# Performance work log

Hardware: AMD Instinct MI355X
Metric: run time of the kernel (lower is better)

Reference implementation:

```python
import jax, jax.numpy as jnp
import numpy as np

N, E = 100000, 1600000
IN, ED, H, HL, OUT = 32, 8, 16, 64, 4
BN_EPS = 1e-5


def setup_inputs() -> dict:
    key = jax.random.key(0)
    keys = iter(jax.random.split(key, 64))

    def rn(*s):
        return jax.random.normal(next(keys), s, jnp.float32) * 0.1

    inp = {}
    inp["x"] = jax.random.normal(next(keys), (N, IN), jnp.float32)
    inp["edge_index"] = jax.random.randint(next(keys), (2, E), 0, N)
    inp["edge_attr"] = jax.random.normal(next(keys), (E, ED), jnp.float32)
    for c, din in ((1, IN), (2, H), (3, H)):
        inp[f"ew{c}"] = rn(ED, din)   # GINEConv edge lin: edge_dim -> in_channels
        inp[f"eb{c}"] = rn(din)
        inp[f"wa{c}"] = rn(din, H)    # nn Linear 1
        inp[f"ba{c}"] = rn(H)
        inp[f"g{c}"] = jnp.ones((H,), jnp.float32)    # BN gamma
        inp[f"be{c}"] = jnp.zeros((H,), jnp.float32)  # BN beta
        inp[f"m{c}"] = rn(H)                           # BN running mean
        inp[f"v{c}"] = jax.random.uniform(next(keys), (H,), jnp.float32, 0.5, 1.5)  # BN running var
        inp[f"wb{c}"] = rn(H, H)      # nn Linear 2
        inp[f"bb{c}"] = rn(H)
    inp["lw1"] = rn(3 * H, HL)
    inp["lb1"] = rn(HL)
    inp["lw2"] = rn(HL, OUT)
    inp["lb2"] = rn(OUT)
    return inp


def gine_conv(x, edge_attr, src, dst, ew, eb, wa, ba, g, be, m, v, wb, bb):
    # message: relu(x_j + lin_edge(edge_attr)); aggregate: sum at dst; eps = 0
    e = edge_attr @ ew + eb                      # [E, din]
    msg = jax.nn.relu(x[src] + e)                # [E, din]
    agg = jax.ops.segment_sum(msg, dst, num_segments=x.shape[0])  # [N, din]
    h = (x + agg) @ wa + ba                      # Linear 1
    h = (h - m) * jax.lax.rsqrt(v + BN_EPS) * g + be  # BatchNorm1d (eval)
    h = jax.nn.relu(h)
    h = jax.nn.relu(h @ wb + bb)                 # Linear 2 + ReLU
    return h


def reference(x, edge_index, edge_attr,
              ew1, eb1, wa1, ba1, g1, be1, m1, v1, wb1, bb1,
              ew2, eb2, wa2, ba2, g2, be2, m2, v2, wb2, bb2,
              ew3, eb3, wa3, ba3, g3, be3, m3, v3, wb3, bb3,
              lw1, lb1, lw2, lb2):
    src, dst = edge_index[0], edge_index[1]
    h1 = gine_conv(x, edge_attr, src, dst, ew1, eb1, wa1, ba1, g1, be1, m1, v1, wb1, bb1)
    h2 = gine_conv(h1, edge_attr, src, dst, ew2, eb2, wa2, ba2, g2, be2, m2, v2, wb2, bb2)
    h3 = gine_conv(h2, edge_attr, src, dst, ew3, eb3, wa3, ba3, g3, be3, m3, v3, wb3, bb3)
    h = jnp.concatenate((h1, h2, h3), axis=1)    # [N, 3H]
    h = jax.nn.relu(h @ lw1 + lb1)               # dropout p=0.5 is identity in eval
    return h @ lw2 + lb2                         # [N, OUT]
```

## Files before the change

kernel.cpp:

```cpp
#include <hip/hip_runtime.h>
#include <hip/hip_bf16.h>

#define BN_EPS 1e-5f
#define BINSHIFT 6
#define BINW 64
#define NBLK 1024

__device__ __forceinline__ unsigned pk_bf16(float x, float y) {
    unsigned ux = __float_as_uint(x);
    ux += 0x7FFFu + ((ux >> 16) & 1u);
    unsigned uy = __float_as_uint(y);
    uy += 0x7FFFu + ((uy >> 16) & 1u);
    return (ux >> 16) | (uy & 0xFFFF0000u);
}
__device__ __forceinline__ float bf_lo(unsigned u) { return __uint_as_float(u << 16); }
__device__ __forceinline__ float bf_hi(unsigned u) { return __uint_as_float(u & 0xFFFF0000u); }

__device__ __forceinline__ int chunk_of(int bid) {
    return ((bid & 7) << 7) | (bid >> 3);
}


__global__ __launch_bounds__(256)
void hist2d_kernel(const int* __restrict__ dst, int* __restrict__ histmat,
                   int E, int nbins, int chunk) {
    __shared__ int h[2048];
    for (int i = threadIdx.x; i < nbins; i += 256) h[i] = 0;
    __syncthreads();
    int c = chunk_of(blockIdx.x);
    int e0 = c * chunk;
    int e1 = min(E, e0 + chunk);
    for (int e = e0 + threadIdx.x; e < e1; e += 256)
        atomicAdd(&h[dst[e] >> BINSHIFT], 1);
    __syncthreads();
    int* row = histmat + (size_t)c * nbins;
    for (int i = threadIdx.x; i < nbins; i += 256) row[i] = h[i];
}

__global__ __launch_bounds__(256)
void colsum_kernel(const int* __restrict__ histmat, int* __restrict__ bincnt,
                   int nbins) {
    int bin = blockIdx.x * 256 + threadIdx.x;
    if (bin >= nbins) return;
    int s = 0;
#pragma unroll 8
    for (int r = 0; r < NBLK; ++r) s += histmat[(size_t)r * nbins + bin];
    bincnt[bin] = s;
}

__global__ __launch_bounds__(1024)
void bin_scan_kernel(const int* __restrict__ bincnt, int* __restrict__ binstart,
                     int nbins, int E) {
    __shared__ int a[2048];
    __shared__ int b[1024];
    int t = threadIdx.x;
    a[t]        = (t < nbins) ? bincnt[t] : 0;
    a[t + 1024] = (t + 1024 < nbins) ? bincnt[t + 1024] : 0;
    __syncthreads();
    b[t] = a[2 * t] + a[2 * t + 1];
    __syncthreads();
    for (int off = 1; off < 1024; off <<= 1) {
        int v = (t >= off) ? b[t - off] : 0;
        __syncthreads();
        b[t] += v;
        __syncthreads();
    }
    int base = (t == 0) ? 0 : b[t - 1];
    if (2 * t < nbins)     binstart[2 * t]     = base;
    if (2 * t + 1 < nbins) binstart[2 * t + 1] = base + a[2 * t];
    if (t == 0) binstart[nbins] = E;
}

__global__ __launch_bounds__(1024)
void rowscan_kernel(int* __restrict__ histmat, const int* __restrict__ binstart,
                    int nbins) {
    __shared__ int a[NBLK];
    int b = blockIdx.x;
    int t = threadIdx.x;
    int v = histmat[(size_t)t * nbins + b];
    a[t] = v;
    __syncthreads();
    for (int off = 1; off < NBLK; off <<= 1) {
        int add = (t >= off) ? a[t - off] : 0;
        __syncthreads();
        a[t] += add;
        __syncthreads();
    }
    histmat[(size_t)t * nbins + b] = binstart[b] + a[t] - v;
}

__global__ __launch_bounds__(256)
void place_kernel(const int* __restrict__ src, const int* __restrict__ dst,
                  const float* __restrict__ edge_attr,
                  const int* __restrict__ histmat,
                  int* __restrict__ tmp_meta, uint4* __restrict__ tmp_ea,
                  int E, int nbins, int chunk) {
    __shared__ int cur[2048];
    int c = chunk_of(blockIdx.x);
    const int* row = histmat + (size_t)c * nbins;
    for (int i = threadIdx.x; i < nbins; i += 256) cur[i] = row[i];
    __syncthreads();
    int e0 = c * chunk;
    int e1 = min(E, e0 + chunk);
    for (int e = e0 + threadIdx.x; e < e1; e += 256) {
        int d = dst[e];
        int bin = d >> BINSHIFT;
        int pos = atomicAdd(&cur[bin], 1);
        tmp_meta[pos] = ((d & (BINW - 1)) << 20) | src[e];
        const float4* sp = (const float4*)(edge_attr + (size_t)e * 8);
        float4 a0 = sp[0], a1 = sp[1];
        uint4 pkd;
        pkd.x = pk_bf16(a0.x, a0.y);
        pkd.y = pk_bf16(a0.z, a0.w);
        pkd.z = pk_bf16(a1.x, a1.y);
        pkd.w = pk_bf16(a1.z, a1.w);
        tmp_ea[pos] = pkd;
    }
}

__global__ __launch_bounds__(256)
void pass2_kernel(const int* __restrict__ binstart, const int* __restrict__ tmp_meta,
                  const uint4* __restrict__ tmp_ea,
                  int* __restrict__ rowstart, int* __restrict__ src_sorted,
                  uint4* __restrict__ ea_sorted, int N, int E) {
    __shared__ int s_cur[BINW];
    int b = blockIdx.x;
    int node0 = b << BINSHIFT;
    int e0 = binstart[b], e1 = binstart[b + 1];
    int t = threadIdx.x;

    if (t < BINW) s_cur[t] = 0;
    __syncthreads();

    for (int e = e0 + t; e < e1; e += 256)
        atomicAdd(&s_cur[tmp_meta[e] >> 20], 1);
    __syncthreads();

    if (t < BINW) {
        int val = s_cur[t];
        int inc = val;
#pragma unroll
        for (int off = 1; off < 64; off <<= 1) {
            int n = __shfl_up(inc, off);
            if (t >= off) inc += n;
        }
        int excl = e0 + inc - val;
        s_cur[t] = excl;
        int node = node0 + t;
        if (node <= N) rowstart[node] = excl;
    }
    __syncthreads();

    for (int e = e0 + t; e < e1; e += 256) {
        int mx = tmp_meta[e];
        int dl   = mx >> 20;
        int srcv = mx & 0xFFFFF;
        int fpos = atomicAdd(&s_cur[dl], 1);
        src_sorted[fpos] = srcv;
        ea_sorted[fpos] = tmp_ea[e];
    }
}

template<int DIN, int C, int S>
__global__ __launch_bounds__(256)
void gine_layer_wave(const float* __restrict__ xin,
                     const int*   __restrict__ rowstart,
                     const int*   __restrict__ src_sorted,
                     const uint4* __restrict__ ea_sorted,
                     const float* __restrict__ ew, const float* __restrict__ eb,
                     const float* __restrict__ wa, const float* __restrict__ ba,
                     const float* __restrict__ g, const float* __restrict__ be,
                     const float* __restrict__ m, const float* __restrict__ v,
                     const float* __restrict__ wb, const float* __restrict__ bb,
                     float* __restrict__ hout,
                     int N) {
    static_assert(C * S == 64 && C * 4 == DIN, "lane layout");
    constexpr int PAD = DIN + 1;

    __shared__ float s_wa[DIN * 16];
    __shared__ float s_wb[256];
    __shared__ float s_ba[16], s_scale[16], s_shift[16], s_bb[16];
    __shared__ float s_s[16 * PAD];
    __shared__ float s_h[16 * 17];

    int t = threadIdx.x;
    for (int idx = t; idx < DIN * 16; idx += 256) s_wa[idx] = wa[idx];
    s_wb[t] = wb[t];
    if (t < 16) {
        s_ba[t] = ba[t];
        float sc = g[t] * rsqrtf(v[t] + BN_EPS);
        s_scale[t] = sc;
        s_shift[t] = be[t] - m[t] * sc;
        s_bb[t] = bb[t];
    }

    int w    = t >> 6;
    int lane = t & 63;
    int c    = lane / S;
    int s    = lane % S;
    int c0   = c * 4;

    float ew_r[8][4];
#pragma unroll
    for (int k = 0; k < 8; ++k) {
        float4 wv = *(const float4*)(ew + k * DIN + c0);
        ew_r[k][0] = wv.x; ew_r[k][1] = wv.y; ew_r[k][2] = wv.z; ew_r[k][3] = wv.w;
    }
    float4 ebv = *(const float4*)(eb + c0);
    float eb_r[4] = {ebv.x, ebv.y, ebv.z, ebv.w};

    int node0 = blockIdx.x * 16;

#pragma unroll
    for (int q = 0; q < 4; ++q) {
        int nl = w * 4 + q;
        int i  = node0 + nl;
        float acc[4] = {0.f, 0.f, 0.f, 0.f};
        if (i < N) {
            int e0 = rowstart[i];
            int e1 = rowstart[i + 1];
            int e  = e0 + s;
            int sv = (e < e1) ? src_sorted[e] : 0;
            for (; e < e1; e += S) {
                int en = e + S;
                int sv_next = (en < e1) ? src_sorted[en] : 0;
                uint4 ev = ea_sorted[e];
                float4 xv = *(const float4*)(xin + (size_t)sv * DIN + c0);
                float av[8] = {bf_lo(ev.x), bf_hi(ev.x), bf_lo(ev.y), bf_hi(ev.y),
                               bf_lo(ev.z), bf_hi(ev.z), bf_lo(ev.w), bf_hi(ev.w)};
                float xr[4] = {xv.x, xv.y, xv.z, xv.w};
#pragma unroll
                for (int j = 0; j < 4; ++j) {
                    float lin = eb_r[j];
#pragma unroll
                    for (int k = 0; k < 8; ++k) lin = fmaf(av[k], ew_r[k][j], lin);
                    lin += xr[j];
                    acc[j] += (lin > 0.f ? lin : 0.f);
                }
                sv = sv_next;
            }
        }
#pragma unroll
        for (int mask = S >> 1; mask >= 1; mask >>= 1) {
#pragma unroll
            for (int j = 0; j < 4; ++j) acc[j] += __shfl_xor(acc[j], mask);
        }
        if (s == 0 && i < N) {
            float4 xi = *(const float4*)(xin + (size_t)i * DIN + c0);
            s_s[nl * PAD + c0 + 0] = acc[0] + xi.x;
            s_s[nl * PAD + c0 + 1] = acc[1] + xi.y;
            s_s[nl * PAD + c0 + 2] = acc[2] + xi.z;
            s_s[nl * PAD + c0 + 3] = acc[3] + xi.w;
        }
    }
    __syncthreads();

    int nl2 = t >> 4;
    int j   = t & 15;
    float a = s_ba[j];
#pragma unroll
    for (int k = 0; k < DIN; ++k)
        a = fmaf(s_s[nl2 * PAD + k], s_wa[k * 16 + j], a);
    a = a * s_scale[j] + s_shift[j];
    s_h[nl2 * 17 + j] = a > 0.f ? a : 0.f;
    __syncthreads();

    float o = s_bb[j];
#pragma unroll
    for (int k = 0; k < 16; ++k)
        o = fmaf(s_h[nl2 * 17 + k], s_wb[k * 16 + j], o);
    o = o > 0.f ? o : 0.f;
    int i2 = node0 + nl2;
    if (i2 < N) hout[(size_t)i2 * 16 + j] = o;
}

__global__ __launch_bounds__(256)
void final_kernel(const float* __restrict__ h1, const float* __restrict__ h2,
                  const float* __restrict__ h3,
                  const float* __restrict__ lw1, const float* __restrict__ lb1,
                  const float* __restrict__ lw2, const float* __restrict__ lb2,
                  float* __restrict__ out, int N) {
    constexpr int NPB = 64;
    __shared__ float s_lw1[48 * 64];
    __shared__ float s_lw2[64 * 4];
    __shared__ float s_lb1[64];
    __shared__ float s_lb2[4];
    __shared__ float s_c[NPB][49];

    int t = threadIdx.x;
    for (int idx = t; idx < 48 * 64; idx += 256) s_lw1[idx] = lw1[idx];
    s_lw2[t] = lw2[t];
    if (t < 64) s_lb1[t] = lb1[t];
    if (t < 4) s_lb2[t] = lb2[t];

    int nl = t >> 2;
    int l  = t & 3;
    int i  = blockIdx.x * NPB + nl;

    if (i < N) {
        float4 c1 = ((const float4*)(h1 + (size_t)i * 16))[l];
        float4 c2 = ((const float4*)(h2 + (size_t)i * 16))[l];
        float4 c3 = ((const float4*)(h3 + (size_t)i * 16))[l];
        s_c[nl][l * 4 + 0] = c1.x; s_c[nl][l * 4 + 1] = c1.y;
        s_c[nl][l * 4 + 2] = c1.z; s_c[nl][l * 4 + 3] = c1.w;
        s_c[nl][16 + l * 4 + 0] = c2.x; s_c[nl][16 + l * 4 + 1] = c2.y;
        s_c[nl][16 + l * 4 + 2] = c2.z; s_c[nl][16 + l * 4 + 3] = c2.w;
        s_c[nl][32 + l * 4 + 0] = c3.x; s_c[nl][32 + l * 4 + 1] = c3.y;
        s_c[nl][32 + l * 4 + 2] = c3.z; s_c[nl][32 + l * 4 + 3] = c3.w;
    }
    __syncthreads();

    float o0 = 0.f, o1 = 0.f, o2 = 0.f, o3 = 0.f;
    if (i < N) {
#pragma unroll 4
        for (int jj = 0; jj < 16; ++jj) {
            int j = l * 16 + jj;
            float a = s_lb1[j];
#pragma unroll
            for (int k = 0; k < 48; ++k) a = fmaf(s_c[nl][k], s_lw1[k * 64 + j], a);
            a = a > 0.f ? a : 0.f;
            o0 = fmaf(a, s_lw2[j * 4 + 0], o0);
            o1 = fmaf(a, s_lw2[j * 4 + 1], o1);
            o2 = fmaf(a, s_lw2[j * 4 + 2], o2);
            o3 = fmaf(a, s_lw2[j * 4 + 3], o3);
        }
    }
    o0 += __shfl_xor(o0, 1); o0 += __shfl_xor(o0, 2);
    o1 += __shfl_xor(o1, 1); o1 += __shfl_xor(o1, 2);
    o2 += __shfl_xor(o2, 1); o2 += __shfl_xor(o2, 2);
    o3 += __shfl_xor(o3, 1); o3 += __shfl_xor(o3, 2);
    if (i < N && l == 0) {
        float4 o = {o0 + s_lb2[0], o1 + s_lb2[1], o2 + s_lb2[2], o3 + s_lb2[3]};
        *(float4*)(out + (size_t)i * 4) = o;
    }
}

extern "C" void kernel_launch(void* const* d_in, const int* in_sizes, int n_in,
                              void* d_out, int out_size, void* d_ws, size_t ws_size,
                              hipStream_t stream) {
    const float* x  = (const float*)d_in[0];
    const int*   ei = (const int*)d_in[1];
    const float* ea = (const float*)d_in[2];
    const int N = in_sizes[0] / 32;
    const int E = in_sizes[1] / 2;
    const int* srci = ei;
    const int* dsti = ei + E;

    const float* lw1 = (const float*)d_in[33];
    const float* lb1 = (const float*)d_in[34];
    const float* lw2 = (const float*)d_in[35];
    const float* lb2 = (const float*)d_in[36];

    const int nbins = (N + BINW - 1) >> BINSHIFT;
    const int chunk = (E + NBLK - 1) / NBLK;

    char* p = (char*)d_ws;
    int*   binstart   = (int*)p;   p += (size_t)(nbins + 1 + 3) / 4 * 16;
    int*   bincnt     = (int*)p;   p += (size_t)(nbins + 3) / 4 * 16;
    int*   rowstart   = (int*)p;   p += (size_t)(N + 1 + 3) / 4 * 16;
    int*   histmat    = (int*)p;   p += (size_t)NBLK * nbins * 4;
    int*   src_sorted = (int*)p;   p += (size_t)E * 4;
    uint4* ea_sorted  = (uint4*)p; p += (size_t)E * 16;
    char*  u          = p;
    int*   tmp_meta   = (int*)u;
    uint4* tmp_ea     = (uint4*)(u + (size_t)E * 4);
    float* h1         = (float*)u;
    float* h2         = h1 + (size_t)N * 16;
    float* h3         = h2 + (size_t)N * 16;

    hist2d_kernel<<<NBLK, 256, 0, stream>>>(dsti, histmat, E, nbins, chunk);
    colsum_kernel<<<(nbins + 255) / 256, 256, 0, stream>>>(histmat, bincnt, nbins);
    bin_scan_kernel<<<1, 1024, 0, stream>>>(bincnt, binstart, nbins, E);
    rowscan_kernel<<<nbins, NBLK, 0, stream>>>(histmat, binstart, nbins);
    place_kernel<<<NBLK, 256, 0, stream>>>(srci, dsti, ea, histmat,
                                           tmp_meta, tmp_ea, E, nbins, chunk);
    pass2_kernel<<<nbins, 256, 0, stream>>>(binstart, tmp_meta, tmp_ea,
                                            rowstart, src_sorted, ea_sorted,
                                            N, E);

    const int lblocks = (N + 15) / 16;
    gine_layer_wave<32, 8, 8><<<lblocks, 256, 0, stream>>>(
        x, rowstart, src_sorted, ea_sorted,
        (const float*)d_in[3], (const float*)d_in[4],
        (const float*)d_in[5], (const float*)d_in[6],
        (const float*)d_in[7], (const float*)d_in[8],
        (const float*)d_in[9], (const float*)d_in[10],
        (const float*)d_in[11], (const float*)d_in[12], h1, N);

    gine_layer_wave<16, 4, 16><<<lblocks, 256, 0, stream>>>(
        h1, rowstart, src_sorted, ea_sorted,
        (const float*)d_in[13], (const float*)d_in[14],
        (const float*)d_in[15], (const float*)d_in[16],
        (const float*)d_in[17], (const float*)d_in[18],
        (const float*)d_in[19], (const float*)d_in[20],
        (const float*)d_in[21], (const float*)d_in[22], h2, N);

    gine_layer_wave<16, 4, 16><<<lblocks, 256, 0, stream>>>(
        h2, rowstart, src_sorted, ea_sorted,
        (const float*)d_in[23], (const float*)d_in[24],
        (const float*)d_in[25], (const float*)d_in[26],
        (const float*)d_in[27], (const float*)d_in[28],
        (const float*)d_in[29], (const float*)d_in[30],
        (const float*)d_in[31], (const float*)d_in[32], h3, N);

    final_kernel<<<(N + 63) / 64, 256, 0, stream>>>(
        h1, h2, h3, lw1, lb1, lw2, lb2, (float*)d_out, N);
}
```

Measured before the change: 519.4 us.

## Transpose block histogram for segmented column scan; store layer outputs as bf16

```diff
diff --git a/kernel.cpp b/kernel.cpp
--- a/kernel.cpp
+++ b/kernel.cpp
@@ -5,6 +5,8 @@
 #define BINSHIFT 6
 #define BINW 64
 #define NBLK 1024
+#define NSEG 8
+#define SEGW (NBLK / NSEG)
 
 __device__ __forceinline__ unsigned pk_bf16(float x, float y) {
     unsigned ux = __float_as_uint(x);
@@ -13,6 +15,14 @@
     uy += 0x7FFFu + ((uy >> 16) & 1u);
     return (ux >> 16) | (uy & 0xFFFF0000u);
 }
+__device__ __forceinline__ unsigned short f2bf(float x) {
+    unsigned u = __float_as_uint(x);
+    u += 0x7FFFu + ((u >> 16) & 1u);
+    return (unsigned short)(u >> 16);
+}
+__device__ __forceinline__ float bfu(unsigned short u) {
+    return __uint_as_float((unsigned)u << 16);
+}
 __device__ __forceinline__ float bf_lo(unsigned u) { return __uint_as_float(u << 16); }
 __device__ __forceinline__ float bf_hi(unsigned u) { return __uint_as_float(u & 0xFFFF0000u); }
 
@@ -22,7 +32,7 @@
 
 
 __global__ __launch_bounds__(256)
-void hist2d_kernel(const int* __restrict__ dst, int* __restrict__ histmat,
+void hist2d_kernel(const int* __restrict__ dst, int* __restrict__ histmatT,
                    int E, int nbins, int chunk) {
     __shared__ int h[2048];
     for (int i = threadIdx.x; i < nbins; i += 256) h[i] = 0;
@@ -33,19 +43,26 @@
     for (int e = e0 + threadIdx.x; e < e1; e += 256)
         atomicAdd(&h[dst[e] >> BINSHIFT], 1);
     __syncthreads();
-    int* row = histmat + (size_t)c * nbins;
-    for (int i = threadIdx.x; i < nbins; i += 256) row[i] = h[i];
-}
-
-__global__ __launch_bounds__(256)
-void colsum_kernel(const int* __restrict__ histmat, int* __restrict__ bincnt,
-                   int nbins) {
+    for (int i = threadIdx.x; i < nbins; i += 256)
+        histmatT[(size_t)i * NBLK + c] = h[i];
+}
+
+__global__ __launch_bounds__(256)
+void colsum_kernel(const int* __restrict__ histmatT, int* __restrict__ bincnt,
+                   int* __restrict__ segsum, int nbins) {
     int bin = blockIdx.x * 256 + threadIdx.x;
     if (bin >= nbins) return;
-    int s = 0;
-#pragma unroll 8
-    for (int r = 0; r < NBLK; ++r) s += histmat[(size_t)r * nbins + bin];
-    bincnt[bin] = s;
+    const int* col = histmatT + (size_t)bin * NBLK;
+    int tot = 0;
+#pragma unroll
+    for (int s = 0; s < NSEG; ++s) {
+        int ps = 0;
+#pragma unroll 16
+        for (int r = 0; r < SEGW; ++r) ps += col[s * SEGW + r];
+        segsum[s * nbins + bin] = ps;
+        tot += ps;
+    }
+    bincnt[bin] = tot;
 }
 
 __global__ __launch_bounds__(1024)
@@ -71,33 +88,33 @@
     if (t == 0) binstart[nbins] = E;
 }
 
-__global__ __launch_bounds__(1024)
-void rowscan_kernel(int* __restrict__ histmat, const int* __restrict__ binstart,
+__global__ __launch_bounds__(256)
+void rowscan_kernel(const int* __restrict__ histmatT, const int* __restrict__ binstart,
+                    const int* __restrict__ segsum, int* __restrict__ basemat,
                     int nbins) {
-    __shared__ int a[NBLK];
-    int b = blockIdx.x;
-    int t = threadIdx.x;
-    int v = histmat[(size_t)t * nbins + b];
-    a[t] = v;
-    __syncthreads();
-    for (int off = 1; off < NBLK; off <<= 1) {
-        int add = (t >= off) ? a[t - off] : 0;
-        __syncthreads();
-        a[t] += add;
-        __syncthreads();
-    }
-    histmat[(size_t)t * nbins + b] = binstart[b] + a[t] - v;
+    int bin = blockIdx.x * 256 + threadIdx.x;
+    if (bin >= nbins) return;
+    int seg = blockIdx.y;
+    int base = binstart[bin];
+    for (int s = 0; s < seg; ++s) base += segsum[s * nbins + bin];
+    const int* col = histmatT + (size_t)bin * NBLK + seg * SEGW;
+#pragma unroll 8
+    for (int r = 0; r < SEGW; ++r) {
+        int v = col[r];
+        basemat[(size_t)(seg * SEGW + r) * nbins + bin] = base;
+        base += v;
+    }
 }
 
 __global__ __launch_bounds__(256)
 void place_kernel(const int* __restrict__ src, const int* __restrict__ dst,
                   const float* __restrict__ edge_attr,
-                  const int* __restrict__ histmat,
+                  const int* __restrict__ basemat,
                   int* __restrict__ tmp_meta, uint4* __restrict__ tmp_ea,
                   int E, int nbins, int chunk) {
     __shared__ int cur[2048];
     int c = chunk_of(blockIdx.x);
-    const int* row = histmat + (size_t)c * nbins;
+    const int* row = basemat + (size_t)c * nbins;
     for (int i = threadIdx.x; i < nbins; i += 256) cur[i] = row[i];
     __syncthreads();
     int e0 = c * chunk;
@@ -161,9 +178,9 @@
     }
 }
 
-template<int DIN, int C, int S>
-__global__ __launch_bounds__(256)
-void gine_layer_wave(const float* __restrict__ xin,
+template<int DIN, int C, int S, bool XBF>
+__global__ __launch_bounds__(256)
+void gine_layer_wave(const void* __restrict__ xin_,
                      const int*   __restrict__ rowstart,
                      const int*   __restrict__ src_sorted,
                      const uint4* __restrict__ ea_sorted,
@@ -172,10 +189,12 @@
                      const float* __restrict__ g, const float* __restrict__ be,
                      const float* __restrict__ m, const float* __restrict__ v,
                      const float* __restrict__ wb, const float* __restrict__ bb,
-                     float* __restrict__ hout,
+                     unsigned short* __restrict__ hout,
                      int N) {
     static_assert(C * S == 64 && C * 4 == DIN, "lane layout");
     constexpr int PAD = DIN + 1;
+    const float* xf = (const float*)xin_;
+    const unsigned short* xb = (const unsigned short*)xin_;
 
     __shared__ float s_wa[DIN * 16];
     __shared__ float s_wb[256];
@@ -225,10 +244,17 @@
                 int en = e + S;
                 int sv_next = (en < e1) ? src_sorted[en] : 0;
                 uint4 ev = ea_sorted[e];
-                float4 xv = *(const float4*)(xin + (size_t)sv * DIN + c0);
+                float xr[4];
+                if constexpr (XBF) {
+                    ushort4 xv = *(const ushort4*)(xb + (size_t)sv * DIN + c0);
+                    xr[0] = bfu(xv.x); xr[1] = bfu(xv.y);
+                    xr[2] = bfu(xv.z); xr[3] = bfu(xv.w);
+                } else {
+                    float4 xv = *(const float4*)(xf + (size_t)sv * DIN + c0);
+                    xr[0] = xv.x; xr[1] = xv.y; xr[2] = xv.z; xr[3] = xv.w;
+                }
                 float av[8] = {bf_lo(ev.x), bf_hi(ev.x), bf_lo(ev.y), bf_hi(ev.y),
                                bf_lo(ev.z), bf_hi(ev.z), bf_lo(ev.w), bf_hi(ev.w)};
-                float xr[4] = {xv.x, xv.y, xv.z, xv.w};
 #pragma unroll
                 for (int j = 0; j < 4; ++j) {
                     float lin = eb_r[j];
@@ -246,11 +272,19 @@
             for (int j = 0; j < 4; ++j) acc[j] += __shfl_xor(acc[j], mask);
         }
         if (s == 0 && i < N) {
-            float4 xi = *(const float4*)(xin + (size_t)i * DIN + c0);
-            s_s[nl * PAD + c0 + 0] = acc[0] + xi.x;
-            s_s[nl * PAD + c0 + 1] = acc[1] + xi.y;
-            s_s[nl * PAD + c0 + 2] = acc[2] + xi.z;
-            s_s[nl * PAD + c0 + 3] = acc[3] + xi.w;
+            float xi[4];
+            if constexpr (XBF) {
+                ushort4 xv = *(const ushort4*)(xb + (size_t)i * DIN + c0);
+                xi[0] = bfu(xv.x); xi[1] = bfu(xv.y);
+                xi[2] = bfu(xv.z); xi[3] = bfu(xv.w);
+            } else {
+                float4 xv = *(const float4*)(xf + (size_t)i * DIN + c0);
+                xi[0] = xv.x; xi[1] = xv.y; xi[2] = xv.z; xi[3] = xv.w;
+            }
+            s_s[nl * PAD + c0 + 0] = acc[0] + xi[0];
+            s_s[nl * PAD + c0 + 1] = acc[1] + xi[1];
+            s_s[nl * PAD + c0 + 2] = acc[2] + xi[2];
+            s_s[nl * PAD + c0 + 3] = acc[3] + xi[3];
         }
     }
     __syncthreads();
@@ -271,12 +305,13 @@
         o = fmaf(s_h[nl2 * 17 + k], s_wb[k * 16 + j], o);
     o = o > 0.f ? o : 0.f;
     int i2 = node0 + nl2;
-    if (i2 < N) hout[(size_t)i2 * 16 + j] = o;
-}
-
-__global__ __launch_bounds__(256)
-void final_kernel(const float* __restrict__ h1, const float* __restrict__ h2,
-                  const float* __restrict__ h3,
+    if (i2 < N) hout[(size_t)i2 * 16 + j] = f2bf(o);
+}
+
+__global__ __launch_bounds__(256)
+void final_kernel(const unsigned short* __restrict__ h1,
+                  const unsigned short* __restrict__ h2,
+                  const unsigned short* __restrict__ h3,
                   const float* __restrict__ lw1, const float* __restrict__ lb1,
                   const float* __restrict__ lw2, const float* __restrict__ lb2,
                   float* __restrict__ out, int N) {
@@ -298,15 +333,15 @@
     int i  = blockIdx.x * NPB + nl;
 
     if (i < N) {
-        float4 c1 = ((const float4*)(h1 + (size_t)i * 16))[l];
-        float4 c2 = ((const float4*)(h2 + (size_t)i * 16))[l];
-        float4 c3 = ((const float4*)(h3 + (size_t)i * 16))[l];
-        s_c[nl][l * 4 + 0] = c1.x; s_c[nl][l * 4 + 1] = c1.y;
-        s_c[nl][l * 4 + 2] = c1.z; s_c[nl][l * 4 + 3] = c1.w;
-        s_c[nl][16 + l * 4 + 0] = c2.x; s_c[nl][16 + l * 4 + 1] = c2.y;
-        s_c[nl][16 + l * 4 + 2] = c2.z; s_c[nl][16 + l * 4 + 3] = c2.w;
-        s_c[nl][32 + l * 4 + 0] = c3.x; s_c[nl][32 + l * 4 + 1] = c3.y;
-        s_c[nl][32 + l * 4 + 2] = c3.z; s_c[nl][32 + l * 4 + 3] = c3.w;
+        ushort4 c1 = *(const ushort4*)(h1 + (size_t)i * 16 + l * 4);
+        ushort4 c2 = *(const ushort4*)(h2 + (size_t)i * 16 + l * 4);
+        ushort4 c3 = *(const ushort4*)(h3 + (size_t)i * 16 + l * 4);
+        s_c[nl][l * 4 + 0] = bfu(c1.x); s_c[nl][l * 4 + 1] = bfu(c1.y);
+        s_c[nl][l * 4 + 2] = bfu(c1.z); s_c[nl][l * 4 + 3] = bfu(c1.w);
+        s_c[nl][16 + l * 4 + 0] = bfu(c2.x); s_c[nl][16 + l * 4 + 1] = bfu(c2.y);
+        s_c[nl][16 + l * 4 + 2] = bfu(c2.z); s_c[nl][16 + l * 4 + 3] = bfu(c2.w);
+        s_c[nl][32 + l * 4 + 0] = bfu(c3.x); s_c[nl][32 + l * 4 + 1] = bfu(c3.y);
+        s_c[nl][32 + l * 4 + 2] = bfu(c3.z); s_c[nl][32 + l * 4 + 3] = bfu(c3.w);
     }
     __syncthreads();
 
@@ -357,29 +392,33 @@
     char* p = (char*)d_ws;
     int*   binstart   = (int*)p;   p += (size_t)(nbins + 1 + 3) / 4 * 16;
     int*   bincnt     = (int*)p;   p += (size_t)(nbins + 3) / 4 * 16;
+    int*   segsum     = (int*)p;   p += (size_t)(NSEG * nbins + 3) / 4 * 16;
     int*   rowstart   = (int*)p;   p += (size_t)(N + 1 + 3) / 4 * 16;
-    int*   histmat    = (int*)p;   p += (size_t)NBLK * nbins * 4;
+    int*   histmatT   = (int*)p;   p += (size_t)NBLK * nbins * 4;
+    int*   basemat    = (int*)p;   p += (size_t)NBLK * nbins * 4;
     int*   src_sorted = (int*)p;   p += (size_t)E * 4;
     uint4* ea_sorted  = (uint4*)p; p += (size_t)E * 16;
     char*  u          = p;
     int*   tmp_meta   = (int*)u;
     uint4* tmp_ea     = (uint4*)(u + (size_t)E * 4);
-    float* h1         = (float*)u;
-    float* h2         = h1 + (size_t)N * 16;
-    float* h3         = h2 + (size_t)N * 16;
-
-    hist2d_kernel<<<NBLK, 256, 0, stream>>>(dsti, histmat, E, nbins, chunk);
-    colsum_kernel<<<(nbins + 255) / 256, 256, 0, stream>>>(histmat, bincnt, nbins);
+    unsigned short* h1 = (unsigned short*)u;
+    unsigned short* h2 = h1 + (size_t)N * 16;
+    unsigned short* h3 = h2 + (size_t)N * 16;
+
+    hist2d_kernel<<<NBLK, 256, 0, stream>>>(dsti, histmatT, E, nbins, chunk);
+    colsum_kernel<<<(nbins + 255) / 256, 256, 0, stream>>>(histmatT, bincnt,
+                                                           segsum, nbins);
     bin_scan_kernel<<<1, 1024, 0, stream>>>(bincnt, binstart, nbins, E);
-    rowscan_kernel<<<nbins, NBLK, 0, stream>>>(histmat, binstart, nbins);
-    place_kernel<<<NBLK, 256, 0, stream>>>(srci, dsti, ea, histmat,
+    rowscan_kernel<<<dim3((nbins + 255) / 256, NSEG), 256, 0, stream>>>(
+        histmatT, binstart, segsum, basemat, nbins);
+    place_kernel<<<NBLK, 256, 0, stream>>>(srci, dsti, ea, basemat,
                                            tmp_meta, tmp_ea, E, nbins, chunk);
     pass2_kernel<<<nbins, 256, 0, stream>>>(binstart, tmp_meta, tmp_ea,
                                             rowstart, src_sorted, ea_sorted,
                                             N, E);
 
     const int lblocks = (N + 15) / 16;
-    gine_layer_wave<32, 8, 8><<<lblocks, 256, 0, stream>>>(
+    gine_layer_wave<32, 8, 8, false><<<lblocks, 256, 0, stream>>>(
         x, rowstart, src_sorted, ea_sorted,
         (const float*)d_in[3], (const float*)d_in[4],
         (const float*)d_in[5], (const float*)d_in[6],
@@ -387,7 +426,7 @@
         (const float*)d_in[9], (const float*)d_in[10],
         (const float*)d_in[11], (const float*)d_in[12], h1, N);
 
-    gine_layer_wave<16, 4, 16><<<lblocks, 256, 0, stream>>>(
+    gine_layer_wave<16, 4, 16, true><<<lblocks, 256, 0, stream>>>(
         h1, rowstart, src_sorted, ea_sorted,
         (const float*)d_in[13], (const float*)d_in[14],
         (const float*)d_in[15], (const float*)d_in[16],
@@ -395,7 +434,7 @@
         (const float*)d_in[19], (const float*)d_in[20],
         (const float*)d_in[21], (const float*)d_in[22], h2, N);
 
-    gine_layer_wave<16, 4, 16><<<lblocks, 256, 0, stream>>>(
+    gine_layer_wave<16, 4, 16, true><<<lblocks, 256, 0, stream>>>(
         h2, rowstart, src_sorted, ea_sorted,
         (const float*)d_in[23], (const float*)d_in[24],
         (const float*)d_in[25], (const float*)d_in[26],
```

New measurement: 503.1 us. -3.2%, faster.
